# Optimization experiments

Measured on AMD Instinct MI355X. Metric: run time of the kernel, lower is better.

## Reference

```python
import jax, jax.numpy as jnp
import numpy as np

S, B, D = 2048, 2, 1024          # seq, batch, hidden
E, K = 64, 2                     # num_experts, top_k
I, SI = 512, 512                 # moe_intermediate, shared_expert_intermediate
CAP = 256                        # per-expert capacity; mean load = S*B*K/E = 128, 256 is >16 sigma -> no drops


def setup_inputs() -> dict:
    key = jax.random.key(0)
    ks = jax.random.split(key, 8)
    sc = lambda d: 1.0 / np.sqrt(d)
    return {
        "hidden_states": jax.random.normal(ks[0], (S, B, D), jnp.float32),
        "router_w": jax.random.normal(ks[1], (E, D), jnp.float32) * sc(D),          # FujiTopKRouter.weight
        "gate_up_proj": jax.random.normal(ks[2], (E, 2 * I, D), jnp.float32) * sc(D),
        "down_proj": jax.random.normal(ks[3], (E, D, I), jnp.float32) * sc(I),
        "sh_gate_w": jax.random.normal(ks[4], (SI, D), jnp.float32) * sc(D),
        "sh_up_w": jax.random.normal(ks[5], (SI, D), jnp.float32) * sc(D),
        "sh_down_w": jax.random.normal(ks[6], (D, SI), jnp.float32) * sc(SI),
        "sh_expert_gate_w": jax.random.normal(ks[7], (1, D), jnp.float32) * sc(D),
    }


def _moe(x, router_w, gate_up_proj, down_proj, sh_gate_w, sh_up_w, sh_down_w, sh_expert_gate_w):
    T = x.shape[0]
    # ---- shared expert (SwiGLU) + sigmoid gate ----
    shared = jnp.dot(jax.nn.silu(x @ sh_gate_w.T) * (x @ sh_up_w.T), sh_down_w.T)
    shared = jax.nn.sigmoid(x @ sh_expert_gate_w.T) * shared                      # [T, D]
    # ---- router: softmax (fp32) -> top-k -> normalize ----
    probs = jax.nn.softmax((x @ router_w.T).astype(jnp.float32), axis=-1)         # [T, E]
    top_w, top_i = jax.lax.top_k(probs, K)                                        # [T, K]
    top_w = top_w / (jnp.sum(top_w, axis=-1, keepdims=True) + 1e-9)
    top_w = top_w.astype(x.dtype)
    # ---- dispatch: permute (token, slot) pairs into fixed-capacity expert buffers ----
    e_f = top_i.reshape(-1)                                                       # [T*K] expert id per pair
    w_f = top_w.reshape(-1)                                                       # [T*K]
    tok = jnp.arange(T * K) // K                                                  # [T*K] source token
    oh = jax.nn.one_hot(e_f, E, dtype=jnp.int32)                                  # [T*K, E]
    pos = jnp.sum(jnp.cumsum(oh, axis=0) * oh, axis=-1) - 1                       # slot within expert
    buf = jnp.zeros((E, CAP, D), x.dtype).at[e_f, pos].set(x[tok])                # [E, C, D]
    # ---- per-expert SwiGLU as batched GEMMs ----
    h = jnp.einsum('ecd,eid->eci', buf, gate_up_proj)                             # [E, C, 2I]
    g, u = jnp.split(h, 2, axis=-1)
    y = jnp.einsum('eci,edi->ecd', jax.nn.silu(g) * u, down_proj)                 # [E, C, D]
    # ---- combine: gather back, weight, scatter-add to tokens ----
    routed = jnp.zeros_like(x).at[tok].add(y[e_f, pos] * w_f[:, None])            # [T, D]
    return shared + routed, probs


def reference(hidden_states, router_w, gate_up_proj, down_proj,
              sh_gate_w, sh_up_w, sh_down_w, sh_expert_gate_w):
    s, b, d = hidden_states.shape
    x = hidden_states.reshape(-1, d)
    out, router_logits = _moe(x, router_w, gate_up_proj, down_proj,
                              sh_gate_w, sh_up_w, sh_down_w, sh_expert_gate_w)
    return out.reshape(s, b, d), router_logits
```

## Files before the change

kernel.cpp:

```cpp
#include <hip/hip_runtime.h>
#include <hip/hip_bf16.h>
#include <stdint.h>

#define T_TOK 4096
#define DDIM  1024
#define NEXP  64
#define IDIM  512
#define SIDIM 512
#define CAP   256

typedef __attribute__((ext_vector_type(4))) float f32x4;
typedef __attribute__((ext_vector_type(8))) short bf16x8;

__device__ __forceinline__ bf16x8 cvt8(f32x4 a, f32x4 b) {
    union { __hip_bfloat162 h[4]; bf16x8 v; } u;
    u.h[0] = __float22bfloat162_rn(make_float2(a[0], a[1]));
    u.h[1] = __float22bfloat162_rn(make_float2(a[2], a[3]));
    u.h[2] = __float22bfloat162_rn(make_float2(b[0], b[1]));
    u.h[3] = __float22bfloat162_rn(make_float2(b[2], b[3]));
    return u.v;
}
__device__ __forceinline__ short f2bs(float f) {
    union { __hip_bfloat16 h; short s; } u; u.h = __float2bfloat16(f); return u.s;
}

__device__ __forceinline__ void gload16(const void* g, void* l) {
    __builtin_amdgcn_global_load_lds((const __attribute__((address_space(1))) void*)g,
                                     (__attribute__((address_space(3))) void*)l, 16, 0, 0);
}

__device__ __forceinline__ bf16x8 frag32(const char* reg0, int row, int s) {
    const char* p = reg0 + row * 128;
    int sw = row & 7;
    f32x4 lo = *(const f32x4*)(p + (((2 * s) ^ sw) << 4));
    f32x4 hi = *(const f32x4*)(p + (((2 * s + 1) ^ sw) << 4));
    return cvt8(lo, hi);
}

__global__ __launch_bounds__(256) void logits_kernel(const float* __restrict__ X,
                                                     const float* __restrict__ RW,
                                                     float* __restrict__ lpart) {
    __shared__ float sX[64 * 33];
    __shared__ float sW[64 * 33];
    int m0 = blockIdx.x * 64;
    int kz = blockIdx.y;
    int kbase = kz * 256;
    int tid = threadIdx.x;
    int tg = tid >> 4;
    int eg = tid & 15;
    float acc[4][4] = {};
    for (int k0 = 0; k0 < 256; k0 += 32) {
        __syncthreads();
#pragma unroll
        for (int i = 0; i < 8; ++i) {
            int idx = i * 256 + tid;
            int r = idx >> 5, c = idx & 31;
            sX[r * 33 + c] = X[(size_t)(m0 + r) * DDIM + kbase + k0 + c];
            sW[r * 33 + c] = RW[(size_t)r * DDIM + kbase + k0 + c];
        }
        __syncthreads();
#pragma unroll 4
        for (int k = 0; k < 32; ++k) {
            float xv[4], wv[4];
#pragma unroll
            for (int i = 0; i < 4; ++i) xv[i] = sX[(tg * 4 + i) * 33 + k];
#pragma unroll
            for (int j = 0; j < 4; ++j) wv[j] = sW[(eg * 4 + j) * 33 + k];
#pragma unroll
            for (int i = 0; i < 4; ++i)
#pragma unroll
                for (int j = 0; j < 4; ++j) acc[i][j] += xv[i] * wv[j];
        }
    }
    float* outp = lpart + (size_t)kz * T_TOK * NEXP;
#pragma unroll
    for (int i = 0; i < 4; ++i)
#pragma unroll
        for (int j = 0; j < 4; ++j)
            outp[(size_t)(m0 + tg * 4 + i) * NEXP + eg * 4 + j] = acc[i][j];
}

__global__ __launch_bounds__(256) void topk_kernel(const float* __restrict__ lpart,
                                                   const float* __restrict__ X,
                                                   const float* __restrict__ SEG,
                                                   float* __restrict__ probs_out,
                                                   int* __restrict__ counts,
                                                   int* __restrict__ tok_slot,
                                                   float* __restrict__ w_slot,
                                                   float* __restrict__ gate_sh) {
    int lane = threadIdx.x & 63;
    int wv   = threadIdx.x >> 6;
    int t    = blockIdx.x * 4 + wv;
    size_t li = (size_t)t * NEXP + lane;
    float l = lpart[li] + lpart[(size_t)T_TOK * NEXP + li]
            + lpart[2 * (size_t)T_TOK * NEXP + li] + lpart[3 * (size_t)T_TOK * NEXP + li];
    float mx = l;
    for (int s = 32; s; s >>= 1) mx = fmaxf(mx, __shfl_xor(mx, s));
    float e = __expf(l - mx);
    float sum = e;
    for (int s = 32; s; s >>= 1) sum += __shfl_xor(sum, s);
    float prob = e / sum;
    probs_out[li] = prob;
    float v = prob; int idx = lane;
    for (int s = 32; s; s >>= 1) {
        float ov = __shfl_xor(v, s); int oi = __shfl_xor(idx, s);
        if (ov > v || (ov == v && oi < idx)) { v = ov; idx = oi; }
    }
    float v1 = v; int i1 = idx;
    v = (lane == i1) ? -1e30f : prob; idx = lane;
    for (int s = 32; s; s >>= 1) {
        float ov = __shfl_xor(v, s); int oi = __shfl_xor(idx, s);
        if (ov > v || (ov == v && oi < idx)) { v = ov; idx = oi; }
    }
    float v2 = v; int i2 = idx;
    float denom = v1 + v2 + 1e-9f;
    if (lane == 0) {
        int s1 = atomicAdd(&counts[i1], 1);
        if (s1 < CAP) { tok_slot[i1 * CAP + s1] = t; w_slot[i1 * CAP + s1] = v1 / denom; }
        int s2 = atomicAdd(&counts[i2], 1);
        if (s2 < CAP) { tok_slot[i2 * CAP + s2] = t; w_slot[i2 * CAP + s2] = v2 / denom; }
    }
    float g = 0.f;
    const float* xr = X + (size_t)t * DDIM + lane * 16;
    const float* sr = SEG + lane * 16;
#pragma unroll
    for (int j = 0; j < 4; ++j) {
        f32x4 xv = *(const f32x4*)(xr + j * 4);
        f32x4 sv = *(const f32x4*)(sr + j * 4);
#pragma unroll
        for (int q = 0; q < 4; ++q) g += xv[q] * sv[q];
    }
    for (int s = 32; s; s >>= 1) g += __shfl_xor(g, s);
    if (lane == 0) gate_sh[t] = 1.f / (1.f + __expf(-g));
}

template <bool EXPERT>
__global__ __launch_bounds__(256, 2) void gateup_kernel(const float* __restrict__ X,
                                                        const float* __restrict__ Wg_base,
                                                        const float* __restrict__ Wu_base,
                                                        const int* __restrict__ counts,
                                                        const int* __restrict__ tok_slot,
                                                        short* __restrict__ act_out) {
    __shared__ char smem[2 * 32768];
    int e  = EXPERT ? blockIdx.z : 0;
    int m0 = blockIdx.y * 128;
    int n0 = blockIdx.x * 64;
    int M;
    const float *Wg, *Wu;
    if (EXPERT) {
        M = counts[e]; if (M > CAP) M = CAP;
        if (m0 >= M) return;
        const float* base = Wg_base + (size_t)e * (2 * IDIM) * DDIM;
        Wg = base; Wu = base + (size_t)IDIM * DDIM;
    } else {
        M = T_TOK; Wg = Wg_base; Wu = Wu_base;
    }
    int tid = threadIdx.x, lane = tid & 63, wv = tid >> 6;
    int wm = wv >> 1, wn = wv & 1;

    int srow8 = tid >> 3;
    int scol  = (tid & 7) ^ (srow8 & 7);
    const float* gp[8];
#pragma unroll
    for (int t = 0; t < 4; ++t) {
        int row = t * 32 + srow8;
        int grow;
        if (EXPERT) {
            int rr = m0 + row; if (rr >= M) rr = M - 1;
            grow = tok_slot[e * CAP + rr];
        } else grow = m0 + row;
        gp[t] = X + (size_t)grow * DDIM + scol * 4;
    }
#pragma unroll
    for (int t = 0; t < 2; ++t) {
        int row = t * 32 + srow8;
        gp[4 + t] = Wg + (size_t)(n0 + row) * DDIM + scol * 4;
        gp[6 + t] = Wu + (size_t)(n0 + row) * DDIM + scol * 4;
    }

    auto issue = [&](int buf) {
        char* lb = smem + buf * 32768 + wv * 1024;
#pragma unroll
        for (int t = 0; t < 8; ++t) {
            gload16(gp[t], lb + t * 4096);
            gp[t] += 32;
        }
    };

    int fm = lane & 15, s = lane >> 4;
    f32x4 accg[4][2] = {}, accu[4][2] = {};
    auto compute = [&](int buf) {
        const char* bb = smem + buf * 32768;
        bf16x8 bg[2], bu[2];
#pragma unroll
        for (int nt = 0; nt < 2; ++nt) {
            int row = wn * 32 + nt * 16 + fm;
            bg[nt] = frag32(bb + 16384, row, s);
            bu[nt] = frag32(bb + 24576, row, s);
        }
#pragma unroll
        for (int mt = 0; mt < 4; ++mt) {
            int row = wm * 64 + mt * 16 + fm;
            bf16x8 a = frag32(bb, row, s);
#pragma unroll
            for (int nt = 0; nt < 2; ++nt) {
                accg[mt][nt] = __builtin_amdgcn_mfma_f32_16x16x32_bf16(a, bg[nt], accg[mt][nt], 0, 0, 0);
                accu[mt][nt] = __builtin_amdgcn_mfma_f32_16x16x32_bf16(a, bu[nt], accu[mt][nt], 0, 0, 0);
            }
        }
    };

    issue(0);
#pragma unroll 1
    for (int kt = 0; kt < 32; kt += 2) {
        __syncthreads();
        issue(1);
        compute(0);
        __syncthreads();
        if (kt + 2 < 32) issue(0);
        compute(1);
    }

    int frow = (lane >> 4) * 4, fcol = lane & 15;
    size_t out_base = EXPERT ? (size_t)e * CAP * IDIM : 0;
#pragma unroll
    for (int mt = 0; mt < 4; ++mt)
#pragma unroll
        for (int r = 0; r < 4; ++r) {
            int row = m0 + wm * 64 + mt * 16 + frow + r;
            if (row < M) {
#pragma unroll
                for (int nt = 0; nt < 2; ++nt) {
                    float g = accg[mt][nt][r];
                    float u = accu[mt][nt][r];
                    float a = (g / (1.f + __expf(-g))) * u;
                    act_out[out_base + (size_t)row * IDIM + (n0 + wn * 32 + nt * 16 + fcol)] = f2bs(a);
                }
            }
        }
}

template <bool EXPERT>
__global__ __launch_bounds__(256, 3) void down_kernel(const short* __restrict__ A_base,
                                                      const float* __restrict__ W_base,
                                                      const int* __restrict__ counts,
                                                      const int* __restrict__ tok_slot,
                                                      const float* __restrict__ w_slot,
                                                      const float* __restrict__ gate_sh,
                                                      float* __restrict__ out) {
    __shared__ char smem[2 * 24576];
    const int KD = IDIM;
    int e  = EXPERT ? blockIdx.z : 0;
    int m0 = blockIdx.y * 128;
    int n0 = blockIdx.x * 128;
    int M;
    const short* A;
    const float* W;
    if (EXPERT) {
        M = counts[e]; if (M > CAP) M = CAP;
        if (m0 >= M) return;
        A = A_base + (size_t)e * CAP * IDIM;
        W = W_base + (size_t)e * DDIM * IDIM;
    } else { M = T_TOK; A = A_base; W = W_base; }
    int tid = threadIdx.x, lane = tid & 63, wv = tid >> 6;
    int wm = wv >> 1, wn = wv & 1;

    const short* ap[2];
#pragma unroll
    for (int t = 0; t < 2; ++t) {
        int row = t * 64 + (tid >> 2);
        int col = (tid & 3) ^ ((tid >> 2) & 3);
        ap[t] = A + (size_t)(m0 + row) * KD + col * 8;
    }
    const float* bp[4];
    {
        int srow8 = tid >> 3;
        int col = (tid & 7) ^ (srow8 & 7);
#pragma unroll
        for (int t = 0; t < 4; ++t) {
            int row = t * 32 + srow8;
            bp[t] = W + (size_t)(n0 + row) * KD + col * 4;
        }
    }

    auto issue = [&](int buf) {
        char* lb = smem + buf * 24576 + wv * 1024;
#pragma unroll
        for (int t = 0; t < 2; ++t) {
            gload16(ap[t], lb + t * 4096);
            ap[t] += 32;
        }
#pragma unroll
        for (int t = 0; t < 4; ++t) {
            gload16(bp[t], lb + 8192 + t * 4096);
            bp[t] += 32;
        }
    };

    int fm = lane & 15, s = lane >> 4;
    f32x4 acc[4][4] = {};
    auto compute = [&](int buf) {
        const char* bb = smem + buf * 24576;
        bf16x8 b[4];
#pragma unroll
        for (int nt = 0; nt < 4; ++nt) {
            int row = wn * 64 + nt * 16 + fm;
            b[nt] = frag32(bb + 8192, row, s);
        }
#pragma unroll
        for (int mt = 0; mt < 4; ++mt) {
            int row = wm * 64 + mt * 16 + fm;
            bf16x8 a = *(const bf16x8*)(bb + row * 64 + ((s ^ (row & 3)) << 4));
#pragma unroll
            for (int nt = 0; nt < 4; ++nt)
                acc[mt][nt] = __builtin_amdgcn_mfma_f32_16x16x32_bf16(a, b[nt], acc[mt][nt], 0, 0, 0);
        }
    };

    issue(0);
#pragma unroll 1
    for (int kt = 0; kt < 16; kt += 2) {
        __syncthreads();
        issue(1);
        compute(0);
        __syncthreads();
        if (kt + 2 < 16) issue(0);
        compute(1);
    }

    int frow = (lane >> 4) * 4, fcol = lane & 15;
#pragma unroll
    for (int mt = 0; mt < 4; ++mt)
#pragma unroll
        for (int r = 0; r < 4; ++r) {
            int row = m0 + wm * 64 + mt * 16 + frow + r;
            if (row >= M) continue;
            float scale; int trow;
            if (EXPERT) { scale = w_slot[e * CAP + row]; trow = tok_slot[e * CAP + row]; }
            else        { scale = gate_sh[row];          trow = row; }
#pragma unroll
            for (int nt = 0; nt < 4; ++nt) {
                int col = n0 + wn * 64 + nt * 16 + fcol;
                float vv = acc[mt][nt][r] * scale;
                if (EXPERT) atomicAdd(&out[(size_t)trow * DDIM + col], vv);
                else        out[(size_t)trow * DDIM + col] = vv;
            }
        }
}

extern "C" void kernel_launch(void* const* d_in, const int* in_sizes, int n_in,
                              void* d_out, int out_size, void* d_ws, size_t ws_size,
                              hipStream_t stream) {
    const float* X   = (const float*)d_in[0];
    const float* RW  = (const float*)d_in[1];
    const float* GUP = (const float*)d_in[2];
    const float* DW  = (const float*)d_in[3];
    const float* SG  = (const float*)d_in[4];
    const float* SU  = (const float*)d_in[5];
    const float* SD  = (const float*)d_in[6];
    const float* SEG = (const float*)d_in[7];
    float* out = (float*)d_out;

    char* ws = (char*)d_ws;
    size_t off = 0;
    float* lpart    = (float*)(ws + off); off += 4 * (size_t)T_TOK * NEXP * 4;
    int*   counts   = (int*)  (ws + off); off += 1024;
    int*   tok_slot = (int*)  (ws + off); off += (size_t)NEXP * CAP * 4;
    float* w_slot   = (float*)(ws + off); off += (size_t)NEXP * CAP * 4;
    float* gate_sh  = (float*)(ws + off); off += (size_t)T_TOK * 4;
    short* act      = (short*)(ws + off); off += (size_t)NEXP * CAP * IDIM * 2;
    short* act_sh   = (short*)(ws + off); off += (size_t)T_TOK * SIDIM * 2;
    (void)ws_size; (void)in_sizes; (void)n_in; (void)out_size;

    hipMemsetAsync(counts, 0, NEXP * sizeof(int), stream);
    logits_kernel<<<dim3(T_TOK / 64, 4), 256, 0, stream>>>(X, RW, lpart);
    topk_kernel<<<T_TOK / 4, 256, 0, stream>>>(lpart, X, SEG,
                                               out + (size_t)T_TOK * DDIM,
                                               counts, tok_slot, w_slot, gate_sh);
    gateup_kernel<false><<<dim3(SIDIM / 64, T_TOK / 128, 1), 256, 0, stream>>>(
        X, SG, SU, nullptr, nullptr, act_sh);
    gateup_kernel<true><<<dim3(IDIM / 64, CAP / 128, NEXP), 256, 0, stream>>>(
        X, GUP, GUP, counts, tok_slot, act);
    down_kernel<false><<<dim3(DDIM / 128, T_TOK / 128, 1), 256, 0, stream>>>(
        act_sh, SD, nullptr, nullptr, nullptr, gate_sh, out);
    down_kernel<true><<<dim3(DDIM / 128, CAP / 128, NEXP), 256, 0, stream>>>(
        act, DW, counts, tok_slot, w_slot, nullptr, out);
}
```

Before: 669.0 us.

## Merge shared and routed expert GEMMs into single launches, deepen router K-split

Measured after the change: 649.2 us. -3.0%, faster.

```diff
diff --git a/kernel.cpp b/kernel.cpp
--- a/kernel.cpp
+++ b/kernel.cpp
@@ -8,6 +8,7 @@
 #define IDIM  512
 #define SIDIM 512
 #define CAP   256
+#define KZ    8
 
 typedef __attribute__((ext_vector_type(4))) float f32x4;
 typedef __attribute__((ext_vector_type(8))) short bf16x8;
@@ -44,12 +45,12 @@
     __shared__ float sW[64 * 33];
     int m0 = blockIdx.x * 64;
     int kz = blockIdx.y;
-    int kbase = kz * 256;
+    int kbase = kz * (DDIM / KZ);
     int tid = threadIdx.x;
     int tg = tid >> 4;
     int eg = tid & 15;
     float acc[4][4] = {};
-    for (int k0 = 0; k0 < 256; k0 += 32) {
+    for (int k0 = 0; k0 < DDIM / KZ; k0 += 32) {
         __syncthreads();
 #pragma unroll
         for (int i = 0; i < 8; ++i) {
@@ -92,8 +93,9 @@
     int wv   = threadIdx.x >> 6;
     int t    = blockIdx.x * 4 + wv;
     size_t li = (size_t)t * NEXP + lane;
-    float l = lpart[li] + lpart[(size_t)T_TOK * NEXP + li]
-            + lpart[2 * (size_t)T_TOK * NEXP + li] + lpart[3 * (size_t)T_TOK * NEXP + li];
+    float l = 0.f;
+#pragma unroll
+    for (int z = 0; z < KZ; ++z) l += lpart[(size_t)z * T_TOK * NEXP + li];
     float mx = l;
     for (int s = 32; s; s >>= 1) mx = fmaxf(mx, __shfl_xor(mx, s));
     float e = __expf(l - mx);
@@ -134,26 +136,36 @@
     if (lane == 0) gate_sh[t] = 1.f / (1.f + __expf(-g));
 }
 
-template <bool EXPERT>
-__global__ __launch_bounds__(256, 2) void gateup_kernel(const float* __restrict__ X,
-                                                        const float* __restrict__ Wg_base,
-                                                        const float* __restrict__ Wu_base,
-                                                        const int* __restrict__ counts,
-                                                        const int* __restrict__ tok_slot,
-                                                        short* __restrict__ act_out) {
+__global__ __launch_bounds__(256, 2) void gateup_all(const float* __restrict__ X,
+                                                     const float* __restrict__ GUP,
+                                                     const float* __restrict__ SG,
+                                                     const float* __restrict__ SU,
+                                                     const int* __restrict__ counts,
+                                                     const int* __restrict__ tok_slot,
+                                                     short* __restrict__ act,
+                                                     short* __restrict__ act_sh) {
     __shared__ char smem[2 * 32768];
-    int e  = EXPERT ? blockIdx.z : 0;
-    int m0 = blockIdx.y * 128;
-    int n0 = blockIdx.x * 64;
-    int M;
+    int f = blockIdx.x;
+    bool expert = f < 1024;
+    int e = 0, m0, n0, M;
     const float *Wg, *Wu;
-    if (EXPERT) {
+    short* act_out;
+    size_t out_base;
+    if (expert) {
+        int r = f & 7, q = (f >> 3) & 7, n = (f >> 6) & 7, y = f >> 9;
+        e = q * 8 + r;
+        n0 = n * 64; m0 = y * 128;
         M = counts[e]; if (M > CAP) M = CAP;
         if (m0 >= M) return;
-        const float* base = Wg_base + (size_t)e * (2 * IDIM) * DDIM;
+        const float* base = GUP + (size_t)e * (2 * IDIM) * DDIM;
         Wg = base; Wu = base + (size_t)IDIM * DDIM;
+        act_out = act; out_base = (size_t)e * CAP * IDIM;
     } else {
-        M = T_TOK; Wg = Wg_base; Wu = Wu_base;
+        int g = f - 1024;
+        int mp = g & 31, n = g >> 5;
+        n0 = n * 64; m0 = mp * 128;
+        M = T_TOK; Wg = SG; Wu = SU;
+        act_out = act_sh; out_base = 0;
     }
     int tid = threadIdx.x, lane = tid & 63, wv = tid >> 6;
     int wm = wv >> 1, wn = wv & 1;
@@ -165,7 +177,7 @@
     for (int t = 0; t < 4; ++t) {
         int row = t * 32 + srow8;
         int grow;
-        if (EXPERT) {
+        if (expert) {
             int rr = m0 + row; if (rr >= M) rr = M - 1;
             grow = tok_slot[e * CAP + rr];
         } else grow = m0 + row;
@@ -222,7 +234,6 @@
     }
 
     int frow = (lane >> 4) * 4, fcol = lane & 15;
-    size_t out_base = EXPERT ? (size_t)e * CAP * IDIM : 0;
 #pragma unroll
     for (int mt = 0; mt < 4; ++mt)
 #pragma unroll
@@ -240,28 +251,36 @@
         }
 }
 
-template <bool EXPERT>
-__global__ __launch_bounds__(256, 3) void down_kernel(const short* __restrict__ A_base,
-                                                      const float* __restrict__ W_base,
-                                                      const int* __restrict__ counts,
-                                                      const int* __restrict__ tok_slot,
-                                                      const float* __restrict__ w_slot,
-                                                      const float* __restrict__ gate_sh,
-                                                      float* __restrict__ out) {
+__global__ __launch_bounds__(256, 3) void down_all(const short* __restrict__ act,
+                                                   const short* __restrict__ act_sh,
+                                                   const float* __restrict__ DW,
+                                                   const float* __restrict__ SD,
+                                                   const int* __restrict__ counts,
+                                                   const int* __restrict__ tok_slot,
+                                                   const float* __restrict__ w_slot,
+                                                   const float* __restrict__ gate_sh,
+                                                   float* __restrict__ out) {
     __shared__ char smem[2 * 24576];
     const int KD = IDIM;
-    int e  = EXPERT ? blockIdx.z : 0;
-    int m0 = blockIdx.y * 128;
-    int n0 = blockIdx.x * 128;
-    int M;
+    int f = blockIdx.x;
+    bool expert = f < 1024;
+    int e = 0, m0, n0, M;
     const short* A;
     const float* W;
-    if (EXPERT) {
+    if (expert) {
+        int r = f & 7, q = (f >> 3) & 7, n = (f >> 6) & 7, y = f >> 9;
+        e = q * 8 + r;
+        n0 = n * 128; m0 = y * 128;
         M = counts[e]; if (M > CAP) M = CAP;
         if (m0 >= M) return;
-        A = A_base + (size_t)e * CAP * IDIM;
-        W = W_base + (size_t)e * DDIM * IDIM;
-    } else { M = T_TOK; A = A_base; W = W_base; }
+        A = act + (size_t)e * CAP * IDIM;
+        W = DW + (size_t)e * DDIM * IDIM;
+    } else {
+        int g = f - 1024;
+        int mp = g & 31, n = g >> 5;
+        n0 = n * 128; m0 = mp * 128;
+        M = T_TOK; A = act_sh; W = SD;
+    }
     int tid = threadIdx.x, lane = tid & 63, wv = tid >> 6;
     int wm = wv >> 1, wn = wv & 1;
 
@@ -336,14 +355,12 @@
             int row = m0 + wm * 64 + mt * 16 + frow + r;
             if (row >= M) continue;
             float scale; int trow;
-            if (EXPERT) { scale = w_slot[e * CAP + row]; trow = tok_slot[e * CAP + row]; }
+            if (expert) { scale = w_slot[e * CAP + row]; trow = tok_slot[e * CAP + row]; }
             else        { scale = gate_sh[row];          trow = row; }
 #pragma unroll
             for (int nt = 0; nt < 4; ++nt) {
                 int col = n0 + wn * 64 + nt * 16 + fcol;
-                float vv = acc[mt][nt][r] * scale;
-                if (EXPERT) atomicAdd(&out[(size_t)trow * DDIM + col], vv);
-                else        out[(size_t)trow * DDIM + col] = vv;
+                atomicAdd(&out[(size_t)trow * DDIM + col], acc[mt][nt][r] * scale);
             }
         }
 }
@@ -363,7 +380,7 @@
 
     char* ws = (char*)d_ws;
     size_t off = 0;
-    float* lpart    = (float*)(ws + off); off += 4 * (size_t)T_TOK * NEXP * 4;
+    float* lpart    = (float*)(ws + off); off += (size_t)KZ * T_TOK * NEXP * 4;
     int*   counts   = (int*)  (ws + off); off += 1024;
     int*   tok_slot = (int*)  (ws + off); off += (size_t)NEXP * CAP * 4;
     float* w_slot   = (float*)(ws + off); off += (size_t)NEXP * CAP * 4;
@@ -373,16 +390,12 @@
     (void)ws_size; (void)in_sizes; (void)n_in; (void)out_size;
 
     hipMemsetAsync(counts, 0, NEXP * sizeof(int), stream);
-    logits_kernel<<<dim3(T_TOK / 64, 4), 256, 0, stream>>>(X, RW, lpart);
+    hipMemsetAsync(out, 0, (size_t)T_TOK * DDIM * sizeof(float), stream);
+    logits_kernel<<<dim3(T_TOK / 64, KZ), 256, 0, stream>>>(X, RW, lpart);
     topk_kernel<<<T_TOK / 4, 256, 0, stream>>>(lpart, X, SEG,
                                                out + (size_t)T_TOK * DDIM,
                                                counts, tok_slot, w_slot, gate_sh);
-    gateup_kernel<false><<<dim3(SIDIM / 64, T_TOK / 128, 1), 256, 0, stream>>>(
-        X, SG, SU, nullptr, nullptr, act_sh);
-    gateup_kernel<true><<<dim3(IDIM / 64, CAP / 128, NEXP), 256, 0, stream>>>(
-        X, GUP, GUP, counts, tok_slot, act);
-    down_kernel<false><<<dim3(DDIM / 128, T_TOK / 128, 1), 256, 0, stream>>>(
-        act_sh, SD, nullptr, nullptr, nullptr, gate_sh, out);
-    down_kernel<true><<<dim3(DDIM / 128, CAP / 128, NEXP), 256, 0, stream>>>(
-        act, DW, counts, tok_slot, w_slot, nullptr, out);
-}
+    gateup_all<<<1280, 256, 0, stream>>>(X, GUP, SG, SU, counts, tok_slot, act, act_sh);
+    down_all<<<1280, 256, 0, stream>>>(act, act_sh, DW, SD, counts, tok_slot,
+                                       w_slot, gate_sh, out);
+}
```
